# Kernel optimization log

Measured on AMD Instinct MI355X. Metric: run time of the kernel, lower is better.

Reference implementation:

```python
import jax, jax.numpy as jnp
import numpy as np

B = 65536
LATENT = 256
POSE_DIM, SHAPE_DIM, ROT_DIM, TRANS_DIM = 15, 10, 3, 3
N_JOINTS = 16  # MANO kinematic tree (wrist + 3 per finger x 5)
PARENTS = (-1, 0, 1, 2, 0, 4, 5, 0, 7, 8, 0, 10, 11, 0, 13, 14)


def setup_inputs() -> dict:
    key = jax.random.key(0)
    ks = jax.random.split(key, 13)
    f32 = jnp.float32
    inp = {
        'z_left': jax.random.normal(ks[0], (B, LATENT), dtype=f32),
        'z_right': jax.random.normal(ks[1], (B, LATENT), dtype=f32),
        # MLP params (Linear(256,512) -> ReLU -> Linear(512,256) -> ReLU -> Linear(256,31))
        'W1': jax.random.normal(ks[2], (LATENT, 512), dtype=f32) * 0.02,
        'b1': jnp.zeros((512,), dtype=f32),
        'W2': jax.random.normal(ks[3], (512, 256), dtype=f32) * 0.02,
        'b2': jnp.zeros((256,), dtype=f32),
        'W3': jax.random.normal(ks[4], (256, 31), dtype=f32) * 0.02,
        'b3': jnp.zeros((31,), dtype=f32),
        # MANO model parameters
        'J_template': jax.random.normal(ks[5], (N_JOINTS, 3), dtype=f32) * 0.05,
        'shape_dirs': jax.random.normal(ks[6], (N_JOINTS, 3, SHAPE_DIM), dtype=f32) * 0.01,
        'hands_components': jax.random.normal(ks[7], (POSE_DIM, 45), dtype=f32) * 0.1,  # PCA -> 15 joints axis-angle
        'hands_mean': jax.random.normal(ks[8], (45,), dtype=f32) * 0.1,
    }
    return inp


def rodrigues(r):
    """Axis-angle [..., 3] -> rotation matrices [..., 3, 3]."""
    theta = jnp.sqrt(jnp.sum(r * r, axis=-1, keepdims=True) + 1e-12)  # [...,1]
    k = r / theta
    kx, ky, kz = k[..., 0], k[..., 1], k[..., 2]
    z = jnp.zeros_like(kx)
    K = jnp.stack([z, -kz, ky, kz, z, -kx, -ky, kx, z], axis=-1)
    K = K.reshape(r.shape[:-1] + (3, 3))
    ct = jnp.cos(theta)[..., None]
    st = jnp.sin(theta)[..., None]
    I = jnp.eye(3, dtype=r.dtype)
    return I + st * K + (1.0 - ct) * (K @ K)


def _decode(z, W1, b1, W2, b2, W3, b3, J_template, shape_dirs, hands_components, hands_mean, is_right):
    # small MLP -> MANO params
    h = jax.nn.relu(z @ W1 + b1)
    h = jax.nn.relu(h @ W2 + b2)
    p = h @ W3 + b3                                    # [B,31]
    pose = p[:, :POSE_DIM]                             # [B,15] PCA coeffs
    shape = p[:, POSE_DIM:POSE_DIM + SHAPE_DIM]        # [B,10]
    rot = p[:, 25:28]                                  # global axis-angle
    trans = p[:, 28:31]

    # shape blend on joint template
    J = J_template[None] + jnp.einsum('jkd,bd->bjk', shape_dirs, shape)  # [B,16,3]
    if not is_right:
        J = J * jnp.asarray([-1.0, 1.0, 1.0], dtype=z.dtype)  # mirror for left hand

    # PCA pose -> per-joint axis-angle -> rotations
    full_pose = hands_mean[None] + pose @ hands_components   # [B,45]
    aa = full_pose.reshape(-1, 15, 3)
    R_global = rodrigues(rot)            # [B,3,3]
    R_local = rodrigues(aa)              # [B,15,3,3]
    R = jnp.concatenate([R_global[:, None], R_local], axis=1)  # [B,16,3,3]

    # batched kinematic chain (fixed 16-joint tree)
    Rw = [R[:, 0]]
    t = [J[:, 0]]
    for i in range(1, N_JOINTS):
        par = PARENTS[i]
        Rw.append(jnp.einsum('bij,bjk->bik', Rw[par], R[:, i]))
        t.append(jnp.einsum('bij,bj->bi', Rw[par], J[:, i] - J[:, par]) + t[par])
    joints = jnp.stack(t, axis=1) + trans[:, None, :]   # [B,16,3]
    return joints


def reference(z_left, z_right, W1, b1, W2, b2, W3, b3, J_template, shape_dirs, hands_components, hands_mean):
    joints_left = _decode(z_left, W1, b1, W2, b2, W3, b3, J_template, shape_dirs, hands_components, hands_mean, is_right=False)
    joints_right = _decode(z_right, W1, b1, W2, b2, W3, b3, J_template, shape_dirs, hands_components, hands_mean, is_right=True)
    return (joints_left, joints_right)
```

## Files before the change

kernel.cpp:

```cpp
#include <hip/hip_runtime.h>
#include <hip/hip_bf16.h>

typedef __attribute__((ext_vector_type(8))) short short8;
typedef __attribute__((ext_vector_type(4))) float f32x4;
typedef unsigned short ushort_t;

#define MFMA16(a,b,c) __builtin_amdgcn_mfma_f32_16x16x32_bf16((a),(b),(c),0,0,0)

__device__ __forceinline__ ushort_t f2bf(float x){
  unsigned int u = __builtin_bit_cast(unsigned int, x);
  unsigned int r = (u + 0x7FFFu + ((u >> 16) & 1u)) >> 16;
  return (ushort_t)r;
}
__device__ __forceinline__ float bf2f(ushort_t h){
  unsigned int u = ((unsigned int)h) << 16;
  return __builtin_bit_cast(float, u);
}

__device__ __forceinline__ void mat3mul(float* C, const float* A, const float* B){
  #pragma unroll
  for (int i = 0; i < 3; i++)
    #pragma unroll
    for (int k = 0; k < 3; k++)
      C[i*3+k] = A[i*3+0]*B[0*3+k] + A[i*3+1]*B[1*3+k] + A[i*3+2]*B[2*3+k];
}
__device__ __forceinline__ void rotp(float* o, const float* A, float x, float y, float z, const float* t){
  o[0] = A[0]*x + A[1]*y + A[2]*z + t[0];
  o[1] = A[3]*x + A[4]*y + A[5]*z + t[1];
  o[2] = A[6]*x + A[7]*y + A[8]*z + t[2];
}

__global__ __launch_bounds__(64) void poison_kernel(float* out, float val){
  if (threadIdx.x == 0 && blockIdx.x == 0) out[0] = val;
}

__global__ __launch_bounds__(256) void preconv_kernel(
    const float* __restrict__ W1, const float* __restrict__ W2, const float* __restrict__ W3,
    ushort_t* __restrict__ W1h, ushort_t* __restrict__ W1l,
    ushort_t* __restrict__ W2h, ushort_t* __restrict__ W2l,
    ushort_t* __restrict__ W3h, ushort_t* __restrict__ W3l)
{
  const int idx = blockIdx.x * 256 + threadIdx.x;
  {
    int j = idx & 7, l = (idx >> 3) & 63, kk = (idx >> 9) & 7, nt = idx >> 12;
    int k = kk*32 + (l >> 4)*8 + j, n = nt*16 + (l & 15);
    float w = W1[k*512 + n];
    ushort_t hi = f2bf(w);
    W1h[idx] = hi; W1l[idx] = f2bf(w - bf2f(hi));
  }
  {
    int j = idx & 7, l = (idx >> 3) & 63, kk = (idx >> 9) & 15, nt = idx >> 13;
    int k = kk*32 + (l >> 4)*8 + j, n = nt*16 + (l & 15);
    float w = W2[k*256 + n];
    ushort_t hi = f2bf(w);
    W2h[idx] = hi; W2l[idx] = f2bf(w - bf2f(hi));
  }
  if (idx < 16384){
    int j = idx & 7, l = (idx >> 3) & 63, kk = (idx >> 9) & 7, nt = idx >> 12;
    int k = kk*32 + (l >> 4)*8 + j, n = nt*16 + (l & 15);
    float w = (nt < 2 && n < 31) ? W3[k*31 + n] : 0.f;
    ushort_t hi = f2bf(w);
    W3h[idx] = hi; W3l[idx] = f2bf(w - bf2f(hi));
  }
}

__global__ __launch_bounds__(256, 3) void fused_kernel(
    const float* __restrict__ zL, const float* __restrict__ zR,
    const ushort_t* __restrict__ W1h, const ushort_t* __restrict__ W1l,
    const ushort_t* __restrict__ W2h, const ushort_t* __restrict__ W2l,
    const ushort_t* __restrict__ W3h, const ushort_t* __restrict__ W3l,
    const float* __restrict__ b1, const float* __restrict__ b2, const float* __restrict__ b3,
    const float* __restrict__ Jt, const float* __restrict__ sd,
    const float* __restrict__ hc, const float* __restrict__ hm,
    float* __restrict__ out)
{
  __shared__ ushort_t regA[2*32*264];
  __shared__ ushort_t regB[2*32*72];
  __shared__ float    plbuf[32*33];
  ushort_t* regAhi = regA;
  ushort_t* regAlo = regA + 32*264;
  ushort_t* regBhi = regB;
  ushort_t* regBlo = regB + 32*72;

  const int tid  = threadIdx.x;
  const int lane = tid & 63;
  const int w    = tid >> 6;
  const int lo   = lane & 15;
  const int g    = lane >> 4;
  const int m0   = blockIdx.x * 32;
  const bool right = (m0 >= 65536);
  const float* zsrc = right ? (zR + (size_t)(m0 - 65536) * 256)
                            : (zL + (size_t)m0 * 256);

  #pragma unroll
  for (int i = 0; i < 8; i++){
    int e = i*1024 + tid*4;
    float4 v = *(const float4*)(zsrc + e);
    int r = e >> 8, c = e & 255;
    ushort_t* dh = &regAhi[r*264 + c];
    ushort_t* dl = &regAlo[r*264 + c];
    float vv[4] = {v.x, v.y, v.z, v.w};
    #pragma unroll
    for (int q = 0; q < 4; q++){
      ushort_t hi = f2bf(vv[q]);
      dh[q] = hi; dl[q] = f2bf(vv[q] - bf2f(hi));
    }
  }
  __syncthreads();

  f32x4 accL2[2][4];
  #pragma unroll
  for (int a = 0; a < 2; a++)
    #pragma unroll
    for (int b = 0; b < 4; b++)
      accL2[a][b] = (f32x4){0.f,0.f,0.f,0.f};

  for (int c = 0; c < 8; c++){
    {
      const int nt = c*4 + w;
      short8 bh[8], bl[8];
      #pragma unroll
      for (int kk = 0; kk < 8; kk++){
        bh[kk] = *(const short8*)(W1h + (size_t)(nt*8 + kk)*512 + lane*8);
        bl[kk] = *(const short8*)(W1l + (size_t)(nt*8 + kk)*512 + lane*8);
      }
      const float bias = b1[nt*16 + lo];
      #pragma unroll
      for (int rt = 0; rt < 2; rt++){
        f32x4 ahh = (f32x4){0.f,0.f,0.f,0.f};
        f32x4 ahl = (f32x4){0.f,0.f,0.f,0.f};
        f32x4 alh = (f32x4){0.f,0.f,0.f,0.f};
        #pragma unroll
        for (int kk = 0; kk < 8; kk++){
          short8 ah = *(const short8*)&regAhi[(rt*16 + lo)*264 + kk*32 + g*8];
          short8 al = *(const short8*)&regAlo[(rt*16 + lo)*264 + kk*32 + g*8];
          ahh = MFMA16(ah, bh[kk], ahh);
          ahl = MFMA16(ah, bl[kk], ahl);
          alh = MFMA16(al, bh[kk], alh);
        }
        #pragma unroll
        for (int i = 0; i < 4; i++){
          float v = fmaxf(ahh[i] + ahl[i] + alh[i] + bias, 0.f);
          ushort_t hi = f2bf(v);
          const int ro = (rt*16 + g*4 + i)*72 + w*16 + lo;
          regBhi[ro] = hi; regBlo[ro] = f2bf(v - bf2f(hi));
        }
      }
    }
    __syncthreads();
    {
      #pragma unroll
      for (int x = 0; x < 2; x++){
        short8 b2h[4], b2l[4];
        #pragma unroll
        for (int q = 0; q < 4; q++){
          b2h[q] = *(const short8*)(W2h + (size_t)((w*4+q)*16 + c*2 + x)*512 + lane*8);
          b2l[q] = *(const short8*)(W2l + (size_t)((w*4+q)*16 + c*2 + x)*512 + lane*8);
        }
        #pragma unroll
        for (int rt = 0; rt < 2; rt++){
          short8 ah = *(const short8*)&regBhi[(rt*16 + lo)*72 + x*32 + g*8];
          short8 al = *(const short8*)&regBlo[(rt*16 + lo)*72 + x*32 + g*8];
          #pragma unroll
          for (int q = 0; q < 4; q++){
            accL2[rt][q] = MFMA16(ah, b2h[q], accL2[rt][q]);
            accL2[rt][q] = MFMA16(ah, b2l[q], accL2[rt][q]);
            accL2[rt][q] = MFMA16(al, b2h[q], accL2[rt][q]);
          }
        }
      }
    }
    __syncthreads();
  }

  #pragma unroll
  for (int rt = 0; rt < 2; rt++){
    #pragma unroll
    for (int q = 0; q < 4; q++){
      const int col = w*64 + q*16 + lo;
      const float bias = b2[col];
      #pragma unroll
      for (int i = 0; i < 4; i++){
        float v = fmaxf(accL2[rt][q][i] + bias, 0.f);
        ushort_t hi = f2bf(v);
        const int ro = (rt*16 + g*4 + i)*264 + col;
        regAhi[ro] = hi; regAlo[ro] = f2bf(v - bf2f(hi));
      }
    }
  }
  __syncthreads();

  {
    const int rw = w & 1, nn = w >> 1;
    f32x4 ahh = (f32x4){0.f,0.f,0.f,0.f};
    f32x4 ahl = (f32x4){0.f,0.f,0.f,0.f};
    f32x4 alh = (f32x4){0.f,0.f,0.f,0.f};
    #pragma unroll
    for (int kk = 0; kk < 8; kk++){
      short8 ah = *(const short8*)&regAhi[(rw*16 + lo)*264 + kk*32 + g*8];
      short8 al = *(const short8*)&regAlo[(rw*16 + lo)*264 + kk*32 + g*8];
      short8 bh = *(const short8*)(W3h + (size_t)(nn*8 + kk)*512 + lane*8);
      short8 bl = *(const short8*)(W3l + (size_t)(nn*8 + kk)*512 + lane*8);
      ahh = MFMA16(ah, bh, ahh);
      ahl = MFMA16(ah, bl, ahl);
      alh = MFMA16(al, bh, alh);
    }
    const int col = nn*16 + lo;
    const float bias = (col < 31) ? b3[col] : 0.f;
    #pragma unroll
    for (int i = 0; i < 4; i++)
      plbuf[(rw*16 + g*4 + i)*33 + col] = ahh[i] + ahl[i] + alh[i] + bias;
  }
  __syncthreads();
  const float* pl = plbuf;

  if (tid < 32){
    const int r = tid;
    float p15[15];
    #pragma unroll
    for (int d = 0; d < 15; d++) p15[d] = pl[r*33 + d];
    float sh[10];
    #pragma unroll
    for (int d = 0; d < 10; d++) sh[d] = pl[r*33 + 15 + d];
    const float trx = pl[r*33+28], tr_y = pl[r*33+29], trz = pl[r*33+30];

    float J[16][3];
    #pragma unroll
    for (int jj = 0; jj < 16; jj++){
      #pragma unroll
      for (int k2 = 0; k2 < 3; k2++){
        float v = Jt[jj*3 + k2];
        #pragma unroll
        for (int d = 0; d < 10; d++) v = fmaf(sd[(jj*3 + k2)*10 + d], sh[d], v);
        J[jj][k2] = v;
      }
    }
    if (!right){
      #pragma unroll
      for (int jj = 0; jj < 16; jj++) J[jj][0] = -J[jj][0];
    }

    auto rod = [](float ax, float ay, float az, float* R){
      float th = sqrtf(ax*ax + ay*ay + az*az + 1e-12f);
      float inv = 1.0f / th;
      float kx = ax*inv, ky = ay*inv, kz = az*inv;
      float st = __sinf(th), ct = __cosf(th);
      float omc = 1.0f - ct;
      R[0] = ct + omc*kx*kx;      R[1] = omc*kx*ky - st*kz;  R[2] = omc*kx*kz + st*ky;
      R[3] = omc*kx*ky + st*kz;   R[4] = ct + omc*ky*ky;     R[5] = omc*ky*kz - st*kx;
      R[6] = omc*kx*kz - st*ky;   R[7] = omc*ky*kz + st*kx;  R[8] = ct + omc*kz*kz;
    };
    auto axis_rod = [&](int j, float* R){
      const int base = 3*(j-1);
      float s0 = hm[base+0], s1 = hm[base+1], s2 = hm[base+2];
      #pragma unroll
      for (int d = 0; d < 15; d++){
        float pv = p15[d];
        s0 = fmaf(pv, hc[d*45 + base+0], s0);
        s1 = fmaf(pv, hc[d*45 + base+1], s1);
        s2 = fmaf(pv, hc[d*45 + base+2], s2);
      }
      rod(s0, s1, s2, R);
    };

    float R0[9];
    rod(pl[r*33+25], pl[r*33+26], pl[r*33+27], R0);

    const size_t ob = (right ? (size_t)3145728 : (size_t)0)
                    + (size_t)(m0 - (right ? 65536 : 0) + r) * 48;
    float t0[3] = {J[0][0], J[0][1], J[0][2]};
    out[ob+0] = t0[0]+trx; out[ob+1] = t0[1]+tr_y; out[ob+2] = t0[2]+trz;
    #pragma unroll
    for (int f = 0; f < 5; f++){
      const int i1 = 3*f+1, i2 = 3*f+2, i3 = 3*f+3;
      float R1[9], R2[9], Rw1[9], Rw2[9], t1[3], t2[3], t3[3];
      axis_rod(i1, R1);
      axis_rod(i2, R2);
      mat3mul(Rw1, R0, R1);
      rotp(t1, R0,  J[i1][0]-J[0][0],  J[i1][1]-J[0][1],  J[i1][2]-J[0][2],  t0);
      mat3mul(Rw2, Rw1, R2);
      rotp(t2, Rw1, J[i2][0]-J[i1][0], J[i2][1]-J[i1][1], J[i2][2]-J[i1][2], t1);
      rotp(t3, Rw2, J[i3][0]-J[i2][0], J[i3][1]-J[i2][1], J[i3][2]-J[i2][2], t2);
      out[ob + i1*3+0] = t1[0]+trx; out[ob + i1*3+1] = t1[1]+tr_y; out[ob + i1*3+2] = t1[2]+trz;
      out[ob + i2*3+0] = t2[0]+trx; out[ob + i2*3+1] = t2[1]+tr_y; out[ob + i2*3+2] = t2[2]+trz;
      out[ob + i3*3+0] = t3[0]+trx; out[ob + i3*3+1] = t3[1]+tr_y; out[ob + i3*3+2] = t3[2]+trz;
    }
  }
}

extern "C" void kernel_launch(void* const* d_in, const int* in_sizes, int n_in,
                              void* d_out, int out_size, void* d_ws, size_t ws_size,
                              hipStream_t stream) {
  const float* zL = (const float*)d_in[0];
  const float* zR = (const float*)d_in[1];
  const float* W1 = (const float*)d_in[2];
  const float* b1 = (const float*)d_in[3];
  const float* W2 = (const float*)d_in[4];
  const float* b2 = (const float*)d_in[5];
  const float* W3 = (const float*)d_in[6];
  const float* b3 = (const float*)d_in[7];
  const float* Jt = (const float*)d_in[8];
  const float* sd = (const float*)d_in[9];
  const float* hc = (const float*)d_in[10];
  const float* hm = (const float*)d_in[11];

  float* out = (float*)d_out;

  if (ws_size < 1114112){
    poison_kernel<<<1, 64, 0, stream>>>(out, 20480.f);
    return;
  }

  ushort_t* W1h = (ushort_t*)d_ws;
  ushort_t* W1l = W1h + 131072;
  ushort_t* W2h = W1l + 131072;
  ushort_t* W2l = W2h + 131072;
  ushort_t* W3h = W2l + 131072;
  ushort_t* W3l = W3h + 16384;

  preconv_kernel<<<512, 256, 0, stream>>>(W1, W2, W3, W1h, W1l, W2h, W2l, W3h, W3l);
  fused_kernel<<<4096, 256, 0, stream>>>(zL, zR, W1h, W1l, W2h, W2l, W3h, W3l,
                                         b1, b2, b3, Jt, sd, hc, hm, out);
}
```

Measured before the change: 269.5 us.

## Software-pipeline weight loads across layer chunks and lower occupancy target

Prefetches the next chunk's W1 fragments into registers while the current W2 MFMAs run, hoists W2 fragment loads ahead of the layer-1 compute, and loads W3 fragments before the layer-2 epilogue. The aim is to hide global-memory latency for the weight streams behind MFMA work. The larger live register set forces the launch-bounds hint down from 3 to 2 waves per SIMD, which cuts occupancy and so leaves less room to hide latency across waves.

```diff
diff --git a/kernel.cpp b/kernel.cpp
--- a/kernel.cpp
+++ b/kernel.cpp
@@ -64,7 +64,7 @@
   }
 }
 
-__global__ __launch_bounds__(256, 3) void fused_kernel(
+__global__ __launch_bounds__(256, 2) void fused_kernel(
     const float* __restrict__ zL, const float* __restrict__ zR,
     const ushort_t* __restrict__ W1h, const ushort_t* __restrict__ W1l,
     const ushort_t* __restrict__ W2h, const ushort_t* __restrict__ W2l,
@@ -92,6 +92,13 @@
   const float* zsrc = right ? (zR + (size_t)(m0 - 65536) * 256)
                             : (zL + (size_t)m0 * 256);
 
+  short8 bh[8], bl[8];
+  #pragma unroll
+  for (int kk = 0; kk < 8; kk++){
+    bh[kk] = *(const short8*)(W1h + (size_t)((0*4 + w)*8 + kk)*512 + lane*8);
+    bl[kk] = *(const short8*)(W1l + (size_t)((0*4 + w)*8 + kk)*512 + lane*8);
+  }
+
   #pragma unroll
   for (int i = 0; i < 8; i++){
     int e = i*1024 + tid*4;
@@ -115,62 +122,114 @@
     for (int b = 0; b < 4; b++)
       accL2[a][b] = (f32x4){0.f,0.f,0.f,0.f};
 
+  #pragma unroll
   for (int c = 0; c < 8; c++){
+    const int nt = c*4 + w;
+    const float bias1 = b1[nt*16 + lo];
+
+    short8 b2h0[4], b2l0[4];
+    #pragma unroll
+    for (int q = 0; q < 4; q++){
+      b2h0[q] = *(const short8*)(W2h + (size_t)((w*4+q)*16 + c*2 + 0)*512 + lane*8);
+      b2l0[q] = *(const short8*)(W2l + (size_t)((w*4+q)*16 + c*2 + 0)*512 + lane*8);
+    }
+
     {
-      const int nt = c*4 + w;
-      short8 bh[8], bl[8];
+      f32x4 ahh = (f32x4){0.f,0.f,0.f,0.f};
+      f32x4 ahl = (f32x4){0.f,0.f,0.f,0.f};
+      f32x4 alh = (f32x4){0.f,0.f,0.f,0.f};
       #pragma unroll
       for (int kk = 0; kk < 8; kk++){
-        bh[kk] = *(const short8*)(W1h + (size_t)(nt*8 + kk)*512 + lane*8);
-        bl[kk] = *(const short8*)(W1l + (size_t)(nt*8 + kk)*512 + lane*8);
-      }
-      const float bias = b1[nt*16 + lo];
-      #pragma unroll
-      for (int rt = 0; rt < 2; rt++){
-        f32x4 ahh = (f32x4){0.f,0.f,0.f,0.f};
-        f32x4 ahl = (f32x4){0.f,0.f,0.f,0.f};
-        f32x4 alh = (f32x4){0.f,0.f,0.f,0.f};
-        #pragma unroll
-        for (int kk = 0; kk < 8; kk++){
-          short8 ah = *(const short8*)&regAhi[(rt*16 + lo)*264 + kk*32 + g*8];
-          short8 al = *(const short8*)&regAlo[(rt*16 + lo)*264 + kk*32 + g*8];
-          ahh = MFMA16(ah, bh[kk], ahh);
-          ahl = MFMA16(ah, bl[kk], ahl);
-          alh = MFMA16(al, bh[kk], alh);
-        }
-        #pragma unroll
-        for (int i = 0; i < 4; i++){
-          float v = fmaxf(ahh[i] + ahl[i] + alh[i] + bias, 0.f);
-          ushort_t hi = f2bf(v);
-          const int ro = (rt*16 + g*4 + i)*72 + w*16 + lo;
-          regBhi[ro] = hi; regBlo[ro] = f2bf(v - bf2f(hi));
-        }
+        short8 ah = *(const short8*)&regAhi[(0*16 + lo)*264 + kk*32 + g*8];
+        short8 al = *(const short8*)&regAlo[(0*16 + lo)*264 + kk*32 + g*8];
+        ahh = MFMA16(ah, bh[kk], ahh);
+        ahl = MFMA16(ah, bl[kk], ahl);
+        alh = MFMA16(al, bh[kk], alh);
+      }
+      #pragma unroll
+      for (int i = 0; i < 4; i++){
+        float v = fmaxf(ahh[i] + ahl[i] + alh[i] + bias1, 0.f);
+        ushort_t hi = f2bf(v);
+        const int ro = (0*16 + g*4 + i)*72 + w*16 + lo;
+        regBhi[ro] = hi; regBlo[ro] = f2bf(v - bf2f(hi));
+      }
+    }
+
+    short8 b2h1[4], b2l1[4];
+    #pragma unroll
+    for (int q = 0; q < 4; q++){
+      b2h1[q] = *(const short8*)(W2h + (size_t)((w*4+q)*16 + c*2 + 1)*512 + lane*8);
+      b2l1[q] = *(const short8*)(W2l + (size_t)((w*4+q)*16 + c*2 + 1)*512 + lane*8);
+    }
+
+    {
+      f32x4 ahh = (f32x4){0.f,0.f,0.f,0.f};
+      f32x4 ahl = (f32x4){0.f,0.f,0.f,0.f};
+      f32x4 alh = (f32x4){0.f,0.f,0.f,0.f};
+      #pragma unroll
+      for (int kk = 0; kk < 8; kk++){
+        short8 ah = *(const short8*)&regAhi[(1*16 + lo)*264 + kk*32 + g*8];
+        short8 al = *(const short8*)&regAlo[(1*16 + lo)*264 + kk*32 + g*8];
+        ahh = MFMA16(ah, bh[kk], ahh);
+        ahl = MFMA16(ah, bl[kk], ahl);
+        alh = MFMA16(al, bh[kk], alh);
+      }
+      #pragma unroll
+      for (int i = 0; i < 4; i++){
+        float v = fmaxf(ahh[i] + ahl[i] + alh[i] + bias1, 0.f);
+        ushort_t hi = f2bf(v);
+        const int ro = (1*16 + g*4 + i)*72 + w*16 + lo;
+        regBhi[ro] = hi; regBlo[ro] = f2bf(v - bf2f(hi));
       }
     }
     __syncthreads();
-    {
-      #pragma unroll
-      for (int x = 0; x < 2; x++){
-        short8 b2h[4], b2l[4];
-        #pragma unroll
-        for (int q = 0; q < 4; q++){
-          b2h[q] = *(const short8*)(W2h + (size_t)((w*4+q)*16 + c*2 + x)*512 + lane*8);
-          b2l[q] = *(const short8*)(W2l + (size_t)((w*4+q)*16 + c*2 + x)*512 + lane*8);
-        }
-        #pragma unroll
-        for (int rt = 0; rt < 2; rt++){
-          short8 ah = *(const short8*)&regBhi[(rt*16 + lo)*72 + x*32 + g*8];
-          short8 al = *(const short8*)&regBlo[(rt*16 + lo)*72 + x*32 + g*8];
-          #pragma unroll
-          for (int q = 0; q < 4; q++){
-            accL2[rt][q] = MFMA16(ah, b2h[q], accL2[rt][q]);
-            accL2[rt][q] = MFMA16(ah, b2l[q], accL2[rt][q]);
-            accL2[rt][q] = MFMA16(al, b2h[q], accL2[rt][q]);
-          }
-        }
+
+    if (c < 7){
+      #pragma unroll
+      for (int kk = 0; kk < 4; kk++){
+        bh[kk] = *(const short8*)(W1h + (size_t)(((c+1)*4 + w)*8 + kk)*512 + lane*8);
+        bl[kk] = *(const short8*)(W1l + (size_t)(((c+1)*4 + w)*8 + kk)*512 + lane*8);
+      }
+    }
+    #pragma unroll
+    for (int rt = 0; rt < 2; rt++){
+      short8 ah = *(const short8*)&regBhi[(rt*16 + lo)*72 + 0*32 + g*8];
+      short8 al = *(const short8*)&regBlo[(rt*16 + lo)*72 + 0*32 + g*8];
+      #pragma unroll
+      for (int q = 0; q < 4; q++){
+        accL2[rt][q] = MFMA16(ah, b2h0[q], accL2[rt][q]);
+        accL2[rt][q] = MFMA16(ah, b2l0[q], accL2[rt][q]);
+        accL2[rt][q] = MFMA16(al, b2h0[q], accL2[rt][q]);
+      }
+    }
+
+    if (c < 7){
+      #pragma unroll
+      for (int kk = 4; kk < 8; kk++){
+        bh[kk] = *(const short8*)(W1h + (size_t)(((c+1)*4 + w)*8 + kk)*512 + lane*8);
+        bl[kk] = *(const short8*)(W1l + (size_t)(((c+1)*4 + w)*8 + kk)*512 + lane*8);
+      }
+    }
+    #pragma unroll
+    for (int rt = 0; rt < 2; rt++){
+      short8 ah = *(const short8*)&regBhi[(rt*16 + lo)*72 + 1*32 + g*8];
+      short8 al = *(const short8*)&regBlo[(rt*16 + lo)*72 + 1*32 + g*8];
+      #pragma unroll
+      for (int q = 0; q < 4; q++){
+        accL2[rt][q] = MFMA16(ah, b2h1[q], accL2[rt][q]);
+        accL2[rt][q] = MFMA16(ah, b2l1[q], accL2[rt][q]);
+        accL2[rt][q] = MFMA16(al, b2h1[q], accL2[rt][q]);
       }
     }
     __syncthreads();
+  }
+
+  const int rw = w & 1, nn = w >> 1;
+  short8 w3h[8], w3l[8];
+  #pragma unroll
+  for (int kk = 0; kk < 8; kk++){
+    w3h[kk] = *(const short8*)(W3h + (size_t)(nn*8 + kk)*512 + lane*8);
+    w3l[kk] = *(const short8*)(W3l + (size_t)(nn*8 + kk)*512 + lane*8);
   }
 
   #pragma unroll
@@ -191,7 +250,6 @@
   __syncthreads();
 
   {
-    const int rw = w & 1, nn = w >> 1;
     f32x4 ahh = (f32x4){0.f,0.f,0.f,0.f};
     f32x4 ahl = (f32x4){0.f,0.f,0.f,0.f};
     f32x4 alh = (f32x4){0.f,0.f,0.f,0.f};
@@ -199,11 +257,9 @@
     for (int kk = 0; kk < 8; kk++){
       short8 ah = *(const short8*)&regAhi[(rw*16 + lo)*264 + kk*32 + g*8];
       short8 al = *(const short8*)&regAlo[(rw*16 + lo)*264 + kk*32 + g*8];
-      short8 bh = *(const short8*)(W3h + (size_t)(nn*8 + kk)*512 + lane*8);
-      short8 bl = *(const short8*)(W3l + (size_t)(nn*8 + kk)*512 + lane*8);
-      ahh = MFMA16(ah, bh, ahh);
-      ahl = MFMA16(ah, bl, ahl);
-      alh = MFMA16(al, bh, alh);
+      ahh = MFMA16(ah, w3h[kk], ahh);
+      ahl = MFMA16(ah, w3l[kk], ahl);
+      alh = MFMA16(al, w3h[kk], alh);
     }
     const int col = nn*16 + lo;
     const float bias = (col < 31) ? b3[col] : 0.f;
```

Result: no change. 269.1 us (-0.1%).

## Keep layer-1 input A fragments in registers instead of shared memory

Applied to the files above, without the earlier changes.

Each wave now loads its z rows straight from global memory into register-resident bf16 hi/lo MFMA fragments, and the shared-memory staging of z plus its barrier are removed. Every wave reloads the full 32x256 tile, so global traffic for z goes up fourfold within a block, but repeated LDS reads inside the layer-1 loop disappear. The fragments take about 64 VGPRs, so launch bounds are relaxed to 2 blocks per CU and the c loop is fully unrolled. This cuts occupancy and may raise register pressure or cause spills.

```diff
diff --git a/kernel.cpp b/kernel.cpp
--- a/kernel.cpp
+++ b/kernel.cpp
@@ -64,7 +64,7 @@
   }
 }
 
-__global__ __launch_bounds__(256, 3) void fused_kernel(
+__global__ __launch_bounds__(256, 2) void fused_kernel(
     const float* __restrict__ zL, const float* __restrict__ zR,
     const ushort_t* __restrict__ W1h, const ushort_t* __restrict__ W1l,
     const ushort_t* __restrict__ W2h, const ushort_t* __restrict__ W2l,
@@ -92,21 +92,26 @@
   const float* zsrc = right ? (zR + (size_t)(m0 - 65536) * 256)
                             : (zL + (size_t)m0 * 256);
 
-  #pragma unroll
-  for (int i = 0; i < 8; i++){
-    int e = i*1024 + tid*4;
-    float4 v = *(const float4*)(zsrc + e);
-    int r = e >> 8, c = e & 255;
-    ushort_t* dh = &regAhi[r*264 + c];
-    ushort_t* dl = &regAlo[r*264 + c];
-    float vv[4] = {v.x, v.y, v.z, v.w};
-    #pragma unroll
-    for (int q = 0; q < 4; q++){
-      ushort_t hi = f2bf(vv[q]);
-      dh[q] = hi; dl[q] = f2bf(vv[q] - bf2f(hi));
-    }
-  }
-  __syncthreads();
+  short8 zfh[16], zfl[16];
+  #pragma unroll
+  for (int rt = 0; rt < 2; rt++){
+    #pragma unroll
+    for (int kk = 0; kk < 8; kk++){
+      const float* src = zsrc + (size_t)(rt*16 + lo)*256 + kk*32 + g*8;
+      float4 v0 = *(const float4*)(src);
+      float4 v1 = *(const float4*)(src + 4);
+      float f[8] = {v0.x,v0.y,v0.z,v0.w,v1.x,v1.y,v1.z,v1.w};
+      short8 h, l;
+      #pragma unroll
+      for (int e = 0; e < 8; e++){
+        ushort_t hi = f2bf(f[e]);
+        h[e] = (short)hi;
+        l[e] = (short)f2bf(f[e] - bf2f(hi));
+      }
+      zfh[rt*8 + kk] = h;
+      zfl[rt*8 + kk] = l;
+    }
+  }
 
   f32x4 accL2[2][4];
   #pragma unroll
@@ -115,6 +120,7 @@
     for (int b = 0; b < 4; b++)
       accL2[a][b] = (f32x4){0.f,0.f,0.f,0.f};
 
+  #pragma unroll
   for (int c = 0; c < 8; c++){
     {
       const int nt = c*4 + w;
@@ -132,11 +138,9 @@
         f32x4 alh = (f32x4){0.f,0.f,0.f,0.f};
         #pragma unroll
         for (int kk = 0; kk < 8; kk++){
-          short8 ah = *(const short8*)&regAhi[(rt*16 + lo)*264 + kk*32 + g*8];
-          short8 al = *(const short8*)&regAlo[(rt*16 + lo)*264 + kk*32 + g*8];
-          ahh = MFMA16(ah, bh[kk], ahh);
-          ahl = MFMA16(ah, bl[kk], ahl);
-          alh = MFMA16(al, bh[kk], alh);
+          ahh = MFMA16(zfh[rt*8+kk], bh[kk], ahh);
+          ahl = MFMA16(zfh[rt*8+kk], bl[kk], ahl);
+          alh = MFMA16(zfl[rt*8+kk], bh[kk], alh);
         }
         #pragma unroll
         for (int i = 0; i < 4; i++){
```

Measured after the change: 509.2 us. +88.9%, slower.

## Enlarge row tile to 48 per block and raise MFMA wave priority

Applied to the files above, without the earlier changes.

Each block now handles 48 rows instead of 32, with boundary clamping for the ragged last tile. Weight fragments loaded from global memory are reused across three row tiles instead of two, which cuts global weight traffic per row. It also unrolls the layer loop and wraps MFMA sections in s_setprio. In exchange it uses more LDS and registers, lowers the occupancy target from 3 to 2 blocks, and leaves two waves idle during the second layer-3 pass.

```diff
diff --git a/kernel.cpp b/kernel.cpp
--- a/kernel.cpp
+++ b/kernel.cpp
@@ -64,7 +64,7 @@
   }
 }
 
-__global__ __launch_bounds__(256, 3) void fused_kernel(
+__global__ __launch_bounds__(256, 2) void fused_kernel(
     const float* __restrict__ zL, const float* __restrict__ zR,
     const ushort_t* __restrict__ W1h, const ushort_t* __restrict__ W1l,
     const ushort_t* __restrict__ W2h, const ushort_t* __restrict__ W2l,
@@ -74,29 +74,32 @@
     const float* __restrict__ hc, const float* __restrict__ hm,
     float* __restrict__ out)
 {
-  __shared__ ushort_t regA[2*32*264];
-  __shared__ ushort_t regB[2*32*72];
-  __shared__ float    plbuf[32*33];
+  __shared__ ushort_t regA[2*48*264];
+  __shared__ ushort_t regB[2*48*72];
+  __shared__ float    plbuf[48*33];
   ushort_t* regAhi = regA;
-  ushort_t* regAlo = regA + 32*264;
+  ushort_t* regAlo = regA + 48*264;
   ushort_t* regBhi = regB;
-  ushort_t* regBlo = regB + 32*72;
+  ushort_t* regBlo = regB + 48*72;
 
   const int tid  = threadIdx.x;
   const int lane = tid & 63;
   const int w    = tid >> 6;
   const int lo   = lane & 15;
   const int g    = lane >> 4;
-  const int m0   = blockIdx.x * 32;
-  const bool right = (m0 >= 65536);
-  const float* zsrc = right ? (zR + (size_t)(m0 - 65536) * 256)
+  const bool right = (blockIdx.x >= 1366);
+  const int mb   = blockIdx.x - (right ? 1366 : 0);
+  const int m0   = mb * 48;
+  const int rows = min(48, 65536 - m0);
+  const float* zsrc = right ? (zR + (size_t)m0 * 256)
                             : (zL + (size_t)m0 * 256);
 
   #pragma unroll
-  for (int i = 0; i < 8; i++){
+  for (int i = 0; i < 12; i++){
     int e = i*1024 + tid*4;
-    float4 v = *(const float4*)(zsrc + e);
     int r = e >> 8, c = e & 255;
+    int rs = (r < rows) ? r : (rows - 1);
+    float4 v = *(const float4*)(zsrc + (size_t)rs*256 + c);
     ushort_t* dh = &regAhi[r*264 + c];
     ushort_t* dl = &regAlo[r*264 + c];
     float vv[4] = {v.x, v.y, v.z, v.w};
@@ -108,13 +111,14 @@
   }
   __syncthreads();
 
-  f32x4 accL2[2][4];
-  #pragma unroll
-  for (int a = 0; a < 2; a++)
+  f32x4 accL2[3][4];
+  #pragma unroll
+  for (int a = 0; a < 3; a++)
     #pragma unroll
     for (int b = 0; b < 4; b++)
       accL2[a][b] = (f32x4){0.f,0.f,0.f,0.f};
 
+  #pragma unroll
   for (int c = 0; c < 8; c++){
     {
       const int nt = c*4 + w;
@@ -126,10 +130,11 @@
       }
       const float bias = b1[nt*16 + lo];
       #pragma unroll
-      for (int rt = 0; rt < 2; rt++){
+      for (int rt = 0; rt < 3; rt++){
         f32x4 ahh = (f32x4){0.f,0.f,0.f,0.f};
         f32x4 ahl = (f32x4){0.f,0.f,0.f,0.f};
         f32x4 alh = (f32x4){0.f,0.f,0.f,0.f};
+        __builtin_amdgcn_s_setprio(1);
         #pragma unroll
         for (int kk = 0; kk < 8; kk++){
           short8 ah = *(const short8*)&regAhi[(rt*16 + lo)*264 + kk*32 + g*8];
@@ -138,6 +143,7 @@
           ahl = MFMA16(ah, bl[kk], ahl);
           alh = MFMA16(al, bh[kk], alh);
         }
+        __builtin_amdgcn_s_setprio(0);
         #pragma unroll
         for (int i = 0; i < 4; i++){
           float v = fmaxf(ahh[i] + ahl[i] + alh[i] + bias, 0.f);
@@ -157,8 +163,9 @@
           b2h[q] = *(const short8*)(W2h + (size_t)((w*4+q)*16 + c*2 + x)*512 + lane*8);
           b2l[q] = *(const short8*)(W2l + (size_t)((w*4+q)*16 + c*2 + x)*512 + lane*8);
         }
-        #pragma unroll
-        for (int rt = 0; rt < 2; rt++){
+        __builtin_amdgcn_s_setprio(1);
+        #pragma unroll
+        for (int rt = 0; rt < 3; rt++){
           short8 ah = *(const short8*)&regBhi[(rt*16 + lo)*72 + x*32 + g*8];
           short8 al = *(const short8*)&regBlo[(rt*16 + lo)*72 + x*32 + g*8];
           #pragma unroll
@@ -168,13 +175,14 @@
             accL2[rt][q] = MFMA16(al, b2h[q], accL2[rt][q]);
           }
         }
+        __builtin_amdgcn_s_setprio(0);
       }
     }
     __syncthreads();
   }
 
   #pragma unroll
-  for (int rt = 0; rt < 2; rt++){
+  for (int rt = 0; rt < 3; rt++){
     #pragma unroll
     for (int q = 0; q < 4; q++){
       const int col = w*64 + q*16 + lo;
@@ -190,31 +198,37 @@
   }
   __syncthreads();
 
-  {
-    const int rw = w & 1, nn = w >> 1;
-    f32x4 ahh = (f32x4){0.f,0.f,0.f,0.f};
-    f32x4 ahl = (f32x4){0.f,0.f,0.f,0.f};
-    f32x4 alh = (f32x4){0.f,0.f,0.f,0.f};
-    #pragma unroll
-    for (int kk = 0; kk < 8; kk++){
-      short8 ah = *(const short8*)&regAhi[(rw*16 + lo)*264 + kk*32 + g*8];
-      short8 al = *(const short8*)&regAlo[(rw*16 + lo)*264 + kk*32 + g*8];
-      short8 bh = *(const short8*)(W3h + (size_t)(nn*8 + kk)*512 + lane*8);
-      short8 bl = *(const short8*)(W3l + (size_t)(nn*8 + kk)*512 + lane*8);
-      ahh = MFMA16(ah, bh, ahh);
-      ahl = MFMA16(ah, bl, ahl);
-      alh = MFMA16(al, bh, alh);
-    }
-    const int col = nn*16 + lo;
-    const float bias = (col < 31) ? b3[col] : 0.f;
-    #pragma unroll
-    for (int i = 0; i < 4; i++)
-      plbuf[(rw*16 + g*4 + i)*33 + col] = ahh[i] + ahl[i] + alh[i] + bias;
+  #pragma unroll
+  for (int pass = 0; pass < 2; pass++){
+    const int jb = (pass == 0) ? w : ((w < 2) ? 4 + w : -1);
+    if (jb >= 0){
+      const int rw = jb >> 1, nn = jb & 1;
+      f32x4 ahh = (f32x4){0.f,0.f,0.f,0.f};
+      f32x4 ahl = (f32x4){0.f,0.f,0.f,0.f};
+      f32x4 alh = (f32x4){0.f,0.f,0.f,0.f};
+      __builtin_amdgcn_s_setprio(1);
+      #pragma unroll
+      for (int kk = 0; kk < 8; kk++){
+        short8 ah = *(const short8*)&regAhi[(rw*16 + lo)*264 + kk*32 + g*8];
+        short8 al = *(const short8*)&regAlo[(rw*16 + lo)*264 + kk*32 + g*8];
+        short8 bh = *(const short8*)(W3h + (size_t)(nn*8 + kk)*512 + lane*8);
+        short8 bl = *(const short8*)(W3l + (size_t)(nn*8 + kk)*512 + lane*8);
+        ahh = MFMA16(ah, bh, ahh);
+        ahl = MFMA16(ah, bl, ahl);
+        alh = MFMA16(al, bh, alh);
+      }
+      __builtin_amdgcn_s_setprio(0);
+      const int col = nn*16 + lo;
+      const float bias = (col < 31) ? b3[col] : 0.f;
+      #pragma unroll
+      for (int i = 0; i < 4; i++)
+        plbuf[(rw*16 + g*4 + i)*33 + col] = ahh[i] + ahl[i] + alh[i] + bias;
+    }
   }
   __syncthreads();
   const float* pl = plbuf;
 
-  if (tid < 32){
+  if (tid < rows){
     const int r = tid;
     float p15[15];
     #pragma unroll
@@ -267,7 +281,7 @@
     rod(pl[r*33+25], pl[r*33+26], pl[r*33+27], R0);
 
     const size_t ob = (right ? (size_t)3145728 : (size_t)0)
-                    + (size_t)(m0 - (right ? 65536 : 0) + r) * 48;
+                    + (size_t)(m0 + r) * 48;
     float t0[3] = {J[0][0], J[0][1], J[0][2]};
     out[ob+0] = t0[0]+trx; out[ob+1] = t0[1]+tr_y; out[ob+2] = t0[2]+trz;
     #pragma unroll
@@ -319,6 +333,6 @@
   ushort_t* W3l = W3h + 16384;
 
   preconv_kernel<<<512, 256, 0, stream>>>(W1, W2, W3, W1h, W1l, W2h, W2l, W3h, W3l);
-  fused_kernel<<<4096, 256, 0, stream>>>(zL, zR, W1h, W1l, W2h, W2l, W3h, W3l,
+  fused_kernel<<<2732, 256, 0, stream>>>(zL, zR, W1h, W1l, W2h, W2l, W3h, W3l,
                                          b1, b2, b3, Jt, sd, hc, hm, out);
 }
```

After: 283.7 us. 5.3% more time.
